# Kernel optimization log

Hardware: AMD Instinct MI355X
Metric: run time of the kernel (lower is better)

The kernel has to match this reference:

```python
import jax, jax.numpy as jnp
import numpy as np

B, D_IN, D_OUT, Q_DIM = 8192, 400, 100, 10


def setup_inputs() -> dict:
    key = jax.random.key(0)
    kx, kw = jax.random.split(key)
    X = jax.random.normal(kx, (B, D_IN, Q_DIM), dtype=jnp.float32)
    # FRMap weight: randn(d_out, d_in) / sqrt(d_in)
    W = jax.random.normal(kw, (D_OUT, D_IN), dtype=jnp.float32) / (D_IN ** 0.5)
    return {"X": X, "W": W}


def reference(X, W):
    # FRMap: Y[b] = W @ X[b]  -> (B, d_out, q)
    Y = jnp.einsum('oi,biq->boq', W, X)
    # ReOrth: reduced QR of each tall-skinny (d_out, q) matrix, keep Q
    Q, _ = jnp.linalg.qr(Y, mode='reduced')  # (B, d_out, q)
    return Q
```

## Files before the change

### kernel.cpp

```cpp
#include <hip/hip_runtime.h>
#include <math.h>

#define BATCHES 8192
#define D_IN    400
#define D_OUT   100
#define QD      10
#define KT      64
#define NKT     7
#define MTILES  7
#define WFSZ    (NKT * MTILES * 2 * 64 * 8)
#define XBW     1280
#define NW      4
#define WCH     512
#define QTR     (7 * WCH)

using bf16x8 = __attribute__((ext_vector_type(8))) short;
using f32x4  = __attribute__((ext_vector_type(4))) float;

template <int CTRL>
__device__ __forceinline__ float dpp_add(float x) {
  int s = __builtin_amdgcn_update_dpp(0, __builtin_bit_cast(int, x),
                                      CTRL, 0xF, 0xF, true);
  return x + __builtin_bit_cast(float, s);
}

__device__ __forceinline__ float wsum64(float x) {
  x = dpp_add<0x111>(x);
  x = dpp_add<0x112>(x);
  x = dpp_add<0x114>(x);
  x = dpp_add<0x118>(x);
  x = dpp_add<0x142>(x);
  x = dpp_add<0x143>(x);
  return __builtin_bit_cast(float,
      __builtin_amdgcn_readlane(__builtin_bit_cast(int, x), 63));
}

__device__ __forceinline__ float lane_bcast(float x, int lane) {
  return __builtin_bit_cast(float,
      __builtin_amdgcn_readlane(__builtin_bit_cast(int, x), lane));
}

__device__ __forceinline__ void gload_lds16(const short* g, short* l) {
  __builtin_amdgcn_global_load_lds(
      (const __attribute__((address_space(1))) void*)g,
      (__attribute__((address_space(3))) void*)l, 16, 0, 0);
}

__global__ __launch_bounds__(256) void wprep_kernel(const float* __restrict__ W,
                                                    short* __restrict__ wfh,
                                                    short* __restrict__ wfl) {
  const int e = blockIdx.x * 256 + threadIdx.x;
  if (e >= WFSZ) return;
  const int j = e & 7, lane = (e >> 3) & 63, ks = (e >> 9) & 1, mtkt = e >> 10;
  const int kt = mtkt / MTILES, mt = mtkt - kt * MTILES;
  const int o = mt * 16 + (lane & 15);
  const int k = kt * KT + ks * 32 + (lane >> 4) * 8 + j;
  const float w = (o < D_OUT && k < D_IN) ? W[o * D_IN + k] : 0.f;
  __bf16 h = (__bf16)w;
  float hf = (float)h;
  __bf16 l = (__bf16)(w - hf);
  wfh[e] = __builtin_bit_cast(short, h);
  wfl[e] = __builtin_bit_cast(short, l);
}

__device__ __forceinline__ void qr_and_store(const f32x4* acc, float* stg,
                                             float* dst, int lane, int col,
                                             int quad) {
  if (col < QD) {
    #pragma unroll
    for (int mt = 0; mt < MTILES; ++mt)
      #pragma unroll
      for (int rr = 0; rr < 4; ++rr) {
        const int o = mt * 16 + quad * 4 + rr;
        if (o < D_OUT) stg[o * QD + col] = acc[mt][rr];
      }
  }
  const int r = lane;
  float a0[QD], a1[QD];
  #pragma unroll
  for (int q = 0; q < QD; ++q) a0[q] = stg[r * QD + q];
  const bool has1 = (r + 64) < D_OUT;
  #pragma unroll
  for (int q = 0; q < QD; ++q) a1[q] = has1 ? stg[(r + 64) * QD + q] : 0.f;

  float v0[QD], v1[QD], tau[QD];
  #pragma unroll
  for (int j = 0; j < QD; ++j) {
    float cj0  = (r >= j) ? a0[j] : 0.f;
    float part = cj0 * cj0 + a1[j] * a1[j];
    float sig  = wsum64(part);
    float alpha = lane_bcast(a0[j], j);
    float nrm  = __builtin_amdgcn_sqrtf(sig);
    float aab  = fabsf(alpha);
    float rn   = __builtin_amdgcn_rcpf(nrm);
    float rd   = __builtin_amdgcn_rcpf(aab + nrm);
    float sgn  = (alpha >= 0.f) ? 1.f : -1.f;
    float tj   = (sig > 0.f) ? (1.f + aab * rn) : 0.f;
    float inv  = (sig > 0.f) ? sgn * rd : 0.f;
    tau[j] = tj;
    v0[j]  = (r == j) ? 1.f : ((r > j) ? a0[j] * inv : 0.f);
    v1[j]  = a1[j] * inv;
    #pragma unroll
    for (int k = j + 1; k < QD; ++k) {
      float p = v0[j] * a0[k] + v1[j] * a1[k];
      float s = wsum64(p) * tj;
      a0[k] -= s * v0[j];
      a1[k] -= s * v1[j];
    }
  }
  float q0[QD], q1[QD];
  #pragma unroll
  for (int c = 0; c < QD; ++c) { q0[c] = (r == c) ? 1.f : 0.f; q1[c] = 0.f; }
  #pragma unroll
  for (int j = QD - 1; j >= 0; --j) {
    #pragma unroll
    for (int c = j; c < QD; ++c) {
      float p = v0[j] * q0[c] + v1[j] * q1[c];
      float s = wsum64(p) * tau[j];
      q0[c] -= s * v0[j];
      q1[c] -= s * v1[j];
    }
  }
  #pragma unroll
  for (int c = 0; c < QD; ++c) stg[r * QD + c] = q0[c];
  if (has1) {
    #pragma unroll
    for (int c = 0; c < QD; ++c) stg[(r + 64) * QD + c] = q1[c];
  }
  const float4* src = (const float4*)stg;
  float4* d4 = (float4*)dst;
  #pragma unroll
  for (int u = r; u < (D_OUT * QD) / 4; u += 64) d4[u] = src[u];
}

__global__ __launch_bounds__(256, 4) void fused_kernel(const float* __restrict__ X,
                                                       const short* __restrict__ wfh,
                                                       const short* __restrict__ wfl,
                                                       float* __restrict__ out) {
  __shared__ __align__(16) float xstg[NW * XBW];
  __shared__ __align__(16) short wtile[2 * QTR];
  const int tid  = threadIdx.x;
  const int lane = tid & 63;
  const int wv   = __builtin_amdgcn_readfirstlane(tid >> 6);
  const long b0  = (long)blockIdx.x * (NW * 2) + wv * 2;
  float* xs = xstg + wv * XBW;
  const int col = lane & 15, quad = lane >> 4;

  f32x4 acc0[MTILES], acc1[MTILES];
  #pragma unroll
  for (int t = 0; t < MTILES; ++t) {
    acc0[t] = (f32x4){0.f, 0.f, 0.f, 0.f};
    acc1[t] = (f32x4){0.f, 0.f, 0.f, 0.f};
  }

  auto wissue = [&](int kt, int ks, const short* pl, int buf) {
    const int m1 = wv;
    const int m2 = (wv < 3) ? wv + 4 : 6;
    gload_lds16(pl + ((long)(kt * MTILES + m1) * 2 + ks) * WCH + lane * 8,
                &wtile[buf * QTR + m1 * WCH]);
    gload_lds16(pl + ((long)(kt * MTILES + m2) * 2 + ks) * WCH + lane * 8,
                &wtile[buf * QTR + m2 * WCH]);
  };

  float4 pre[5];
  auto xpre = [&](int kt) {
    const int nk0 = kt * KT;
    const int vf4 = (nk0 + KT <= D_IN) ? 160 : ((D_IN - nk0) * QD) / 4;
    #pragma unroll
    for (int u = 0; u < 5; ++u) {
      const int idx = lane + u * 64;
      const int bsel = idx >= 160 ? 1 : 0;
      const int within = idx - bsel * 160;
      float4 v = {0.f, 0.f, 0.f, 0.f};
      if (within < vf4)
        v = *(const float4*)(X + (b0 + bsel) * (long)(D_IN * QD) + nk0 * QD + within * 4);
      pre[u] = v;
    }
  };
  auto xcommit = [&]() {
    #pragma unroll
    for (int u = 0; u < 5; ++u) {
      const int idx = lane + u * 64;
      *(float4*)&xs[idx * 4] = pre[u];
    }
  };

  bf16x8 b0h, b0l, b1h, b1l;
  auto buildFrags = [&](int ks) {
    #pragma unroll
    for (int m = 0; m < 8; ++m) {
      const int fo = (ks * 32 + quad * 8 + m) * QD + col;
      float x0 = xs[fo];
      float x1 = xs[640 + fo];
      __bf16 h0 = (__bf16)x0; float f0 = (float)h0; __bf16 g0 = (__bf16)(x0 - f0);
      __bf16 h1 = (__bf16)x1; float f1 = (float)h1; __bf16 g1 = (__bf16)(x1 - f1);
      b0h[m] = __builtin_bit_cast(short, h0); b0l[m] = __builtin_bit_cast(short, g0);
      b1h[m] = __builtin_bit_cast(short, h1); b1l[m] = __builtin_bit_cast(short, g1);
    }
  };
  auto computeHi = [&](int buf) {
    #pragma unroll
    for (int mt = 0; mt < MTILES; ++mt) {
      bf16x8 ah = *(const bf16x8*)&wtile[buf * QTR + mt * WCH + lane * 8];
      acc0[mt] = __builtin_amdgcn_mfma_f32_16x16x32_bf16(ah, b0h, acc0[mt], 0, 0, 0);
      acc0[mt] = __builtin_amdgcn_mfma_f32_16x16x32_bf16(ah, b0l, acc0[mt], 0, 0, 0);
      acc1[mt] = __builtin_amdgcn_mfma_f32_16x16x32_bf16(ah, b1h, acc1[mt], 0, 0, 0);
      acc1[mt] = __builtin_amdgcn_mfma_f32_16x16x32_bf16(ah, b1l, acc1[mt], 0, 0, 0);
    }
  };
  auto computeLo = [&](int buf) {
    #pragma unroll
    for (int mt = 0; mt < MTILES; ++mt) {
      bf16x8 al = *(const bf16x8*)&wtile[buf * QTR + mt * WCH + lane * 8];
      acc0[mt] = __builtin_amdgcn_mfma_f32_16x16x32_bf16(al, b0h, acc0[mt], 0, 0, 0);
      acc1[mt] = __builtin_amdgcn_mfma_f32_16x16x32_bf16(al, b1h, acc1[mt], 0, 0, 0);
    }
  };

  wissue(0, 0, wfh, 0);
  __builtin_amdgcn_sched_barrier(0);
  xpre(0);
  __builtin_amdgcn_sched_barrier(0);

  #pragma unroll 1
  for (int kt = 0; kt < NKT; ++kt) {
    xcommit();
    buildFrags(0);
    asm volatile("s_waitcnt vmcnt(0)" ::: "memory");
    __builtin_amdgcn_s_barrier();
    __builtin_amdgcn_sched_barrier(0);
    wissue(kt, 0, wfl, 1);
    computeHi(0);
    asm volatile("s_waitcnt vmcnt(0)" ::: "memory");
    __builtin_amdgcn_s_barrier();
    __builtin_amdgcn_sched_barrier(0);
    wissue(kt, 1, wfh, 0);
    computeLo(1);
    asm volatile("s_waitcnt vmcnt(0)" ::: "memory");
    __builtin_amdgcn_s_barrier();
    __builtin_amdgcn_sched_barrier(0);
    buildFrags(1);
    wissue(kt, 1, wfl, 1);
    __builtin_amdgcn_sched_barrier(0);
    if (kt + 1 < NKT) xpre(kt + 1);
    computeHi(0);
    if (kt + 1 < NKT)
      asm volatile("s_waitcnt vmcnt(5)" ::: "memory");
    else
      asm volatile("s_waitcnt vmcnt(0)" ::: "memory");
    __builtin_amdgcn_s_barrier();
    __builtin_amdgcn_sched_barrier(0);
    if (kt + 1 < NKT) wissue(kt + 1, 0, wfh, 0);
    computeLo(1);
  }

  qr_and_store(acc0, xs, out + b0 * (long)(D_OUT * QD), lane, col, quad);
  qr_and_store(acc1, xs, out + (b0 + 1) * (long)(D_OUT * QD), lane, col, quad);
}

extern "C" void kernel_launch(void* const* d_in, const int* in_sizes, int n_in,
                              void* d_out, int out_size, void* d_ws, size_t ws_size,
                              hipStream_t stream) {
  const float* X = (const float*)d_in[0];
  const float* W = (const float*)d_in[1];
  float* out = (float*)d_out;
  short* wfh = (short*)d_ws;
  short* wfl = wfh + WFSZ;
  hipLaunchKernelGGL(wprep_kernel, dim3((WFSZ + 255) / 256), dim3(256), 0, stream,
                     W, wfh, wfl);
  hipLaunchKernelGGL(fused_kernel, dim3(BATCHES / (NW * 2)), dim3(256), 0, stream,
                     X, wfh, wfl, out);
}
```

Baseline: 258.4 us.

## Load X tiles directly to LDS asynchronously and restage QR panels

Replaces the register-staged X prefetch (global load into registers, then LDS store) with direct global_load_lds into the per-wave X staging area. The loop schedule is reordered so the next W-hi and X tiles are issued before the final computeLo, with vmcnt waits tuned to overlap the loads. Shared memory becomes a single buffer that is reused at the end to stage both output panels before the two QR factorizations run. The goal is to free VGPRs and hide X load latency behind MFMA work. The cost is more barriers and a dependence on correct vmcnt counts. For the tail tile, lanes past the valid range now reload the tile's first elements instead of zeros, which could put stray values into the padded K region unless W is zero there.

```diff
diff --git a/kernel.cpp b/kernel.cpp
--- a/kernel.cpp
+++ b/kernel.cpp
@@ -9,10 +9,12 @@
 #define NKT     7
 #define MTILES  7
 #define WFSZ    (NKT * MTILES * 2 * 64 * 8)
-#define XBW     1280
 #define NW      4
 #define WCH     512
 #define QTR     (7 * WCH)
+#define XWF     1280
+#define SMEMF   (NW * XWF + QTR)
+#define QRSTR   2176
 
 using bf16x8 = __attribute__((ext_vector_type(8))) short;
 using f32x4  = __attribute__((ext_vector_type(4))) float;
@@ -40,7 +42,7 @@
       __builtin_amdgcn_readlane(__builtin_bit_cast(int, x), lane));
 }
 
-__device__ __forceinline__ void gload_lds16(const short* g, short* l) {
+__device__ __forceinline__ void gload_lds16(const void* g, void* l) {
   __builtin_amdgcn_global_load_lds(
       (const __attribute__((address_space(1))) void*)g,
       (__attribute__((address_space(3))) void*)l, 16, 0, 0);
@@ -63,9 +65,8 @@
   wfl[e] = __builtin_bit_cast(short, l);
 }
 
-__device__ __forceinline__ void qr_and_store(const f32x4* acc, float* stg,
-                                             float* dst, int lane, int col,
-                                             int quad) {
+__device__ __forceinline__ void stage_panel(const f32x4* acc, float* stg,
+                                            int col, int quad) {
   if (col < QD) {
     #pragma unroll
     for (int mt = 0; mt < MTILES; ++mt)
@@ -75,6 +76,9 @@
         if (o < D_OUT) stg[o * QD + col] = acc[mt][rr];
       }
   }
+}
+
+__device__ __forceinline__ void qr_from_stg(float* stg, float* dst, int lane) {
   const int r = lane;
   float a0[QD], a1[QD];
   #pragma unroll
@@ -137,13 +141,13 @@
                                                        const short* __restrict__ wfh,
                                                        const short* __restrict__ wfl,
                                                        float* __restrict__ out) {
-  __shared__ __align__(16) float xstg[NW * XBW];
-  __shared__ __align__(16) short wtile[2 * QTR];
+  __shared__ __align__(16) float smem[SMEMF];
   const int tid  = threadIdx.x;
   const int lane = tid & 63;
   const int wv   = __builtin_amdgcn_readfirstlane(tid >> 6);
   const long b0  = (long)blockIdx.x * (NW * 2) + wv * 2;
-  float* xs = xstg + wv * XBW;
+  float* xs = smem + wv * XWF;
+  short* wt = (short*)(smem + NW * XWF);
   const int col = lane & 15, quad = lane >> 4;
 
   f32x4 acc0[MTILES], acc1[MTILES];
@@ -157,31 +161,22 @@
     const int m1 = wv;
     const int m2 = (wv < 3) ? wv + 4 : 6;
     gload_lds16(pl + ((long)(kt * MTILES + m1) * 2 + ks) * WCH + lane * 8,
-                &wtile[buf * QTR + m1 * WCH]);
+                wt + buf * QTR + m1 * WCH);
     gload_lds16(pl + ((long)(kt * MTILES + m2) * 2 + ks) * WCH + lane * 8,
-                &wtile[buf * QTR + m2 * WCH]);
-  };
-
-  float4 pre[5];
-  auto xpre = [&](int kt) {
-    const int nk0 = kt * KT;
-    const int vf4 = (nk0 + KT <= D_IN) ? 160 : ((D_IN - nk0) * QD) / 4;
+                wt + buf * QTR + m2 * WCH);
+  };
+
+  auto xissue = [&](int kt) {
+    const int nk0 = kt * KT * QD;
+    const int vf4 = (kt == NKT - 1) ? 40 : 160;
     #pragma unroll
     for (int u = 0; u < 5; ++u) {
       const int idx = lane + u * 64;
       const int bsel = idx >= 160 ? 1 : 0;
-      const int within = idx - bsel * 160;
-      float4 v = {0.f, 0.f, 0.f, 0.f};
-      if (within < vf4)
-        v = *(const float4*)(X + (b0 + bsel) * (long)(D_IN * QD) + nk0 * QD + within * 4);
-      pre[u] = v;
-    }
-  };
-  auto xcommit = [&]() {
-    #pragma unroll
-    for (int u = 0; u < 5; ++u) {
-      const int idx = lane + u * 64;
-      *(float4*)&xs[idx * 4] = pre[u];
+      int within = idx - bsel * 160;
+      if (within >= vf4) within = 0;
+      gload_lds16(X + (b0 + bsel) * (long)(D_IN * QD) + nk0 + within * 4,
+                  (char*)xs + u * 1024);
     }
   };
 
@@ -201,7 +196,7 @@
   auto computeHi = [&](int buf) {
     #pragma unroll
     for (int mt = 0; mt < MTILES; ++mt) {
-      bf16x8 ah = *(const bf16x8*)&wtile[buf * QTR + mt * WCH + lane * 8];
+      bf16x8 ah = *(const bf16x8*)(wt + buf * QTR + mt * WCH + lane * 8);
       acc0[mt] = __builtin_amdgcn_mfma_f32_16x16x32_bf16(ah, b0h, acc0[mt], 0, 0, 0);
       acc0[mt] = __builtin_amdgcn_mfma_f32_16x16x32_bf16(ah, b0l, acc0[mt], 0, 0, 0);
       acc1[mt] = __builtin_amdgcn_mfma_f32_16x16x32_bf16(ah, b1h, acc1[mt], 0, 0, 0);
@@ -211,7 +206,7 @@
   auto computeLo = [&](int buf) {
     #pragma unroll
     for (int mt = 0; mt < MTILES; ++mt) {
-      bf16x8 al = *(const bf16x8*)&wtile[buf * QTR + mt * WCH + lane * 8];
+      bf16x8 al = *(const bf16x8*)(wt + buf * QTR + mt * WCH + lane * 8);
       acc0[mt] = __builtin_amdgcn_mfma_f32_16x16x32_bf16(al, b0h, acc0[mt], 0, 0, 0);
       acc1[mt] = __builtin_amdgcn_mfma_f32_16x16x32_bf16(al, b1h, acc1[mt], 0, 0, 0);
     }
@@ -219,17 +214,19 @@
 
   wissue(0, 0, wfh, 0);
   __builtin_amdgcn_sched_barrier(0);
-  xpre(0);
+  xissue(0);
+  __builtin_amdgcn_sched_barrier(0);
+  asm volatile("s_waitcnt vmcnt(5)" ::: "memory");
+  __builtin_amdgcn_s_barrier();
   __builtin_amdgcn_sched_barrier(0);
 
   #pragma unroll 1
   for (int kt = 0; kt < NKT; ++kt) {
-    xcommit();
+    wissue(kt, 0, wfl, 1);
+    __builtin_amdgcn_sched_barrier(0);
+    asm volatile("s_waitcnt vmcnt(2)" ::: "memory");
+    __builtin_amdgcn_sched_barrier(0);
     buildFrags(0);
-    asm volatile("s_waitcnt vmcnt(0)" ::: "memory");
-    __builtin_amdgcn_s_barrier();
-    __builtin_amdgcn_sched_barrier(0);
-    wissue(kt, 0, wfl, 1);
     computeHi(0);
     asm volatile("s_waitcnt vmcnt(0)" ::: "memory");
     __builtin_amdgcn_s_barrier();
@@ -239,23 +236,35 @@
     asm volatile("s_waitcnt vmcnt(0)" ::: "memory");
     __builtin_amdgcn_s_barrier();
     __builtin_amdgcn_sched_barrier(0);
+    wissue(kt, 1, wfl, 1);
     buildFrags(1);
-    wissue(kt, 1, wfl, 1);
-    __builtin_amdgcn_sched_barrier(0);
-    if (kt + 1 < NKT) xpre(kt + 1);
     computeHi(0);
+    asm volatile("s_waitcnt vmcnt(0)" ::: "memory");
+    __builtin_amdgcn_s_barrier();
+    __builtin_amdgcn_sched_barrier(0);
+    if (kt + 1 < NKT) {
+      wissue(kt + 1, 0, wfh, 0);
+      __builtin_amdgcn_sched_barrier(0);
+      xissue(kt + 1);
+      __builtin_amdgcn_sched_barrier(0);
+    }
+    computeLo(1);
     if (kt + 1 < NKT)
       asm volatile("s_waitcnt vmcnt(5)" ::: "memory");
     else
       asm volatile("s_waitcnt vmcnt(0)" ::: "memory");
     __builtin_amdgcn_s_barrier();
     __builtin_amdgcn_sched_barrier(0);
-    if (kt + 1 < NKT) wissue(kt + 1, 0, wfh, 0);
-    computeLo(1);
-  }
-
-  qr_and_store(acc0, xs, out + b0 * (long)(D_OUT * QD), lane, col, quad);
-  qr_and_store(acc1, xs, out + (b0 + 1) * (long)(D_OUT * QD), lane, col, quad);
+  }
+
+  float* stgA = smem + wv * QRSTR;
+  float* stgB = stgA + 1024;
+  stage_panel(acc0, stgA, col, quad);
+  stage_panel(acc1, stgB, col, quad);
+  __builtin_amdgcn_sched_barrier(0);
+  qr_from_stg(stgA, out + b0 * (long)(D_OUT * QD), lane);
+  __builtin_amdgcn_sched_barrier(0);
+  qr_from_stg(stgB, out + (b0 + 1) * (long)(D_OUT * QD), lane);
 }
 
 extern "C" void kernel_launch(void* const* d_in, const int* in_sizes, int n_in,
```

New measurement: 232.0 us. -10.2%, faster.
